# Kernel optimization log

Measured on AMD Instinct MI355X. Metric: run time of the kernel, lower is better.

## Reference

```python
import jax, jax.numpy as jnp
import numpy as np

NEG_INF = -9e15
ALPHA = 2.0  # LeakyReLU negative slope from init (alpha=2)


def setup_inputs() -> dict:
    key = jax.random.key(0)
    k1, k2, k3, k4 = jax.random.split(key, 4)
    B, N, Fin, Fout = 8, 2048, 256, 128
    x = jax.random.normal(k1, (B, N, Fin), dtype=jnp.float32)
    adj = jax.random.randint(k2, (B, N, N), 0, 2, dtype=jnp.int32)
    # xavier_uniform with gain=1.414
    def xavier(k, shape, gain=1.414):
        fan_in, fan_out = shape[0], shape[1]
        bound = gain * np.sqrt(6.0 / (fan_in + fan_out))
        return jax.random.uniform(k, shape, jnp.float32, -bound, bound)
    W = xavier(k3, (Fin, Fout))
    a = xavier(k4, (2 * Fout, 1))
    return {"x": x, "adj": adj, "W": W, "a": a}


def reference(x, adj, W, a):
    # Wh: [B, N, Fout]
    Wh = jnp.matmul(x, W)
    Fout = W.shape[1]
    a1 = a[:Fout, 0]   # [Fout]
    a2 = a[Fout:, 0]   # [Fout]
    f1 = jnp.einsum('bnf,f->bn', Wh, a1)  # [B, N]
    f2 = jnp.einsum('bnf,f->bn', Wh, a2)  # [B, N]
    e = f1[:, :, None] + f2[:, None, :]   # [B, N, N]
    e = jnp.where(e >= 0, e, ALPHA * e)   # leaky relu, slope 2
    e = jnp.where(adj > 0, e, NEG_INF)
    attention = jax.nn.softmax(e, axis=2)
    # dropout: eval mode (no-op)
    h_prime = jnp.matmul(attention, Wh)   # [B, N, Fout]
    # concat=True -> elu
    return jnp.where(h_prime > 0, h_prime, jnp.expm1(h_prime))
```

## Files before the change

kernel.cpp:

```cpp
#include <hip/hip_runtime.h>
#include <hip/hip_bf16.h>
#include <math.h>

#define NEGINF (-9000000000000000.0f)

constexpr int B_   = 8;
constexpr int N_   = 2048;
constexpr int FIN  = 256;
constexpr int FOUT = 128;

constexpr int CH  = 512;
constexpr int NCH = N_ / CH;
constexpr int PR  = CH + 8;
constexpr int XR  = FIN + 8;
constexpr int TR  = 40;

typedef __attribute__((ext_vector_type(8))) short bf16x8;
typedef __attribute__((ext_vector_type(4))) float f32x4;

static __device__ __forceinline__ unsigned short f2bf(float f) {
    __hip_bfloat16 h = __float2bfloat16(f);
    return *reinterpret_cast<unsigned short*>(&h);
}

__global__ __launch_bounds__(256) void k0_wt(const float* __restrict__ W,
                                             unsigned short* __restrict__ Wt) {
    const int n = blockIdx.x;
    const int k = threadIdx.x;
    Wt[n * FIN + k] = f2bf(W[k * FOUT + n]);
}

__global__ __launch_bounds__(256) void kadj(const int* __restrict__ adj,
                                            unsigned long long* __restrict__ mask) {
    const int tid  = threadIdx.x;
    const int wave = tid >> 6, lane = tid & 63;
    const size_t row = (size_t)blockIdx.x * 4 + wave;
    const int* src = adj + row * N_;
    unsigned long long* dst = mask + row * (N_ / 64);
#pragma unroll
    for (int g = 0; g < 4; ++g) {
        unsigned long long m[8];
#pragma unroll
        for (int q = 0; q < 8; ++q)
            m[q] = __ballot(src[g * 512 + q * 64 + lane] > 0);
        unsigned long long v = m[0];
#pragma unroll
        for (int q = 1; q < 8; ++q) v = (lane == q) ? m[q] : v;
        if (lane < 8) dst[g * 8 + lane] = v;
    }
}

__global__ __launch_bounds__(256) void ka_wh(const float* __restrict__ x,
                                             const unsigned short* __restrict__ Wt,
                                             const float* __restrict__ a,
                                             unsigned short* __restrict__ WhT,
                                             float* __restrict__ f1,
                                             float* __restrict__ f2) {
    __shared__ unsigned short xs[32 * XR];
    __shared__ float as[2 * FOUT];
    __shared__ float fred[2][4][32];

    const int tid = threadIdx.x;
    const int j0  = blockIdx.x * 32;
    const int b   = j0 >> 11;
    const int jb  = j0 & (N_ - 1);

    if (tid < 2 * FOUT) as[tid] = a[tid];
    {
        const float4* xsrc = (const float4*)(x + (size_t)j0 * FIN);
#pragma unroll
        for (int t = 0; t < 8; ++t) {
            const int idx = tid + t * 256;
            float4 v = xsrc[idx];
            const int row = idx >> 6, c4 = idx & 63;
            ushort4 u;
            u.x = f2bf(v.x); u.y = f2bf(v.y); u.z = f2bf(v.z); u.w = f2bf(v.w);
            *(ushort4*)&xs[row * XR + c4 * 4] = u;
        }
    }
    __syncthreads();

    const int wave = tid >> 6, lane = tid & 63;
    const int quad = lane >> 4, l16 = lane & 15;

    f32x4 acc[2][2];
#pragma unroll
    for (int aa = 0; aa < 2; ++aa)
#pragma unroll
        for (int nn = 0; nn < 2; ++nn) acc[aa][nn] = {0.f, 0.f, 0.f, 0.f};

    const unsigned short* wtA0 = Wt + (size_t)(32 * wave + l16) * FIN;
    const unsigned short* wtA1 = wtA0 + 16 * FIN;
#pragma unroll
    for (int ks = 0; ks < FIN / 32; ++ks) {
        const int kof = ks * 32 + quad * 8;
        bf16x8 af0 = *(const bf16x8*)&wtA0[kof];
        bf16x8 af1 = *(const bf16x8*)&wtA1[kof];
        bf16x8 bf0 = *(const bf16x8*)&xs[l16 * XR + kof];
        bf16x8 bf1 = *(const bf16x8*)&xs[(16 + l16) * XR + kof];
        acc[0][0] = __builtin_amdgcn_mfma_f32_16x16x32_bf16(af0, bf0, acc[0][0], 0, 0, 0);
        acc[0][1] = __builtin_amdgcn_mfma_f32_16x16x32_bf16(af0, bf1, acc[0][1], 0, 0, 0);
        acc[1][0] = __builtin_amdgcn_mfma_f32_16x16x32_bf16(af1, bf0, acc[1][0], 0, 0, 0);
        acc[1][1] = __builtin_amdgcn_mfma_f32_16x16x32_bf16(af1, bf1, acc[1][1], 0, 0, 0);
    }
    __syncthreads();

    unsigned short* T = xs;
    float pf[2][2] = {{0.f, 0.f}, {0.f, 0.f}};
#pragma unroll
    for (int aa = 0; aa < 2; ++aa)
#pragma unroll
        for (int nn = 0; nn < 2; ++nn)
#pragma unroll
            for (int r = 0; r < 4; ++r) {
                const int d = 32 * wave + 16 * aa + 4 * quad + r;
                const float v = acc[aa][nn][r];
                T[d * TR + nn * 16 + l16] = f2bf(v);
                pf[0][nn] += v * as[d];
                pf[1][nn] += v * as[FOUT + d];
            }
#pragma unroll
    for (int ff = 0; ff < 2; ++ff)
#pragma unroll
        for (int nn = 0; nn < 2; ++nn) {
            float v = pf[ff][nn];
            v += __shfl_xor(v, 16);
            v += __shfl_xor(v, 32);
            pf[ff][nn] = v;
        }
    if (quad == 0) {
#pragma unroll
        for (int ff = 0; ff < 2; ++ff)
#pragma unroll
            for (int nn = 0; nn < 2; ++nn)
                fred[ff][wave][nn * 16 + l16] = pf[ff][nn];
    }
    __syncthreads();

    unsigned short* dstW = WhT + (size_t)b * FOUT * N_;
#pragma unroll
    for (int it = 0; it < 2; ++it) {
        const int idx = it * 256 + tid;
        const int d = idx >> 2, q = idx & 3;
        bf16x8 v = *(const bf16x8*)&T[d * TR + q * 8];
        *(bf16x8*)&dstW[(size_t)d * N_ + jb + q * 8] = v;
    }
    if (tid < 64) {
        const int ff = tid >> 5, j32 = tid & 31;
        const float s = fred[ff][0][j32] + fred[ff][1][j32] +
                        fred[ff][2][j32] + fred[ff][3][j32];
        (ff ? f2 : f1)[(size_t)b * N_ + jb + j32] = s;
    }
}

__global__ __launch_bounds__(256) void kb_attn(const unsigned int* __restrict__ mask32,
                                               const unsigned short* __restrict__ WhT,
                                               const float* __restrict__ f1,
                                               const float* __restrict__ f2,
                                               float* __restrict__ out) {
    __shared__ unsigned short p[16 * PR];
    __shared__ float alpha_s[16];
    __shared__ float rsum[16];

    const int tid  = threadIdx.x;
    const int b    = blockIdx.x & 7;
    const int i0   = (blockIdx.x >> 3) * 16;
    const int wave = tid >> 6, lane = tid & 63;
    const int quad = lane >> 4, l16 = lane & 15;

    const float4* f2b4 = (const float4*)(f2 + (size_t)b * N_);

    float f1r[4], m_run[4], s_run[4];
#pragma unroll
    for (int rr = 0; rr < 4; ++rr) {
        f1r[rr]   = f1[(size_t)b * N_ + i0 + wave * 4 + rr];
        m_run[rr] = NEGINF;
        s_run[rr] = 0.f;
    }

    f32x4 acc0 = {0.f, 0.f, 0.f, 0.f}, acc1 = {0.f, 0.f, 0.f, 0.f};
    const int n0 = wave * 32;
    const unsigned short* wB0 = WhT + (size_t)b * FOUT * N_ + (size_t)(n0 + l16) * N_;
    const unsigned short* wB1 = wB0 + (size_t)16 * N_;
    const unsigned short* pA  = &p[l16 * PR];

    for (int c = 0; c < NCH; ++c) {
#pragma unroll
        for (int rr = 0; rr < 4; ++rr) {
            const int ti = wave * 4 + rr;
            const int i  = i0 + ti;
            const float f1i = f1r[rr];
            const unsigned int* mrow =
                mask32 + ((size_t)b * N_ + i) * (N_ / 32);
            const unsigned int w0 = mrow[c * 16 + (lane >> 3)];
            const unsigned int w1 = mrow[c * 16 + 8 + (lane >> 3)];
            const unsigned int t0 = (w0 >> ((lane & 7) * 4)) & 0xF;
            const unsigned int t1 = (w1 >> ((lane & 7) * 4)) & 0xF;
            const int c4 = c * (CH / 4);
            float4 fv0 = f2b4[c4 + lane];
            float4 fv1 = f2b4[c4 + 64 + lane];

            float e[8];
            e[0] = f1i + fv0.x; e[1] = f1i + fv0.y; e[2] = f1i + fv0.z; e[3] = f1i + fv0.w;
            e[4] = f1i + fv1.x; e[5] = f1i + fv1.y; e[6] = f1i + fv1.z; e[7] = f1i + fv1.w;
#pragma unroll
            for (int q = 0; q < 8; ++q) e[q] = (e[q] >= 0.f) ? e[q] : 2.f * e[q];
#pragma unroll
            for (int q = 0; q < 4; ++q) {
                if (!((t0 >> q) & 1)) e[q]     = NEGINF;
                if (!((t1 >> q) & 1)) e[4 + q] = NEGINF;
            }

            float mx = e[0];
#pragma unroll
            for (int q = 1; q < 8; ++q) mx = fmaxf(mx, e[q]);
#pragma unroll
            for (int o = 32; o; o >>= 1) mx = fmaxf(mx, __shfl_xor(mx, o));

            const float mnew = fmaxf(m_run[rr], mx);
            const float al   = __expf(m_run[rr] - mnew);
            float pv[8];
            float s8 = 0.f;
#pragma unroll
            for (int q = 0; q < 8; ++q) { pv[q] = __expf(e[q] - mnew); s8 += pv[q]; }
#pragma unroll
            for (int o = 32; o; o >>= 1) s8 += __shfl_xor(s8, o);
            s_run[rr] = s_run[rr] * al + s8;
            m_run[rr] = mnew;

            ushort4 u0, u1;
            u0.x = f2bf(pv[0]); u0.y = f2bf(pv[1]); u0.z = f2bf(pv[2]); u0.w = f2bf(pv[3]);
            u1.x = f2bf(pv[4]); u1.y = f2bf(pv[5]); u1.z = f2bf(pv[6]); u1.w = f2bf(pv[7]);
            *(ushort4*)&p[ti * PR + 4 * lane]       = u0;
            *(ushort4*)&p[ti * PR + 256 + 4 * lane] = u1;
            if (lane == 0) alpha_s[ti] = al;
            if (c == NCH - 1 && lane == 0) rsum[ti] = s_run[rr];
        }
        __syncthreads();

#pragma unroll
        for (int r = 0; r < 4; ++r) {
            const float alr = alpha_s[quad * 4 + r];
            acc0[r] *= alr;
            acc1[r] *= alr;
        }
        const int kbase = c * CH;
#pragma unroll
        for (int ks = 0; ks < CH / 32; ++ks) {
            const int kof = ks * 32 + quad * 8;
            bf16x8 afr = *(const bf16x8*)&pA[kof];
            bf16x8 b0  = *(const bf16x8*)&wB0[kbase + kof];
            bf16x8 b1  = *(const bf16x8*)&wB1[kbase + kof];
            acc0 = __builtin_amdgcn_mfma_f32_16x16x32_bf16(afr, b0, acc0, 0, 0, 0);
            acc1 = __builtin_amdgcn_mfma_f32_16x16x32_bf16(afr, b1, acc1, 0, 0, 0);
        }
        __syncthreads();
    }

#pragma unroll
    for (int r = 0; r < 4; ++r) {
        const int m = quad * 4 + r;
        const float inv = 1.f / rsum[m];
        float v0 = acc0[r] * inv;
        float v1 = acc1[r] * inv;
        v0 = (v0 > 0.f) ? v0 : expm1f(v0);
        v1 = (v1 > 0.f) ? v1 : expm1f(v1);
        const size_t base = ((size_t)b * N_ + i0 + m) * FOUT + n0;
        out[base + l16]      = v0;
        out[base + 16 + l16] = v1;
    }
}

extern "C" void kernel_launch(void* const* d_in, const int* in_sizes, int n_in,
                              void* d_out, int out_size, void* d_ws, size_t ws_size,
                              hipStream_t stream) {
    const float* x   = (const float*)d_in[0];
    const int*   adj = (const int*)d_in[1];
    const float* W   = (const float*)d_in[2];
    const float* a   = (const float*)d_in[3];
    float* out = (float*)d_out;

    unsigned short* WhT = (unsigned short*)d_ws;
    unsigned short* Wt  = WhT + (size_t)B_ * FOUT * N_;
    float* f1 = (float*)(Wt + (size_t)FOUT * FIN);
    float* f2 = f1 + (size_t)B_ * N_;
    unsigned long long* mask = (unsigned long long*)(f2 + (size_t)B_ * N_);

    hipLaunchKernelGGL(kadj, dim3(B_ * N_ / 4), dim3(256), 0, stream, adj, mask);
    hipLaunchKernelGGL(k0_wt, dim3(FOUT), dim3(FIN), 0, stream, W, Wt);
    hipLaunchKernelGGL(ka_wh, dim3(B_ * N_ / 32), dim3(256), 0, stream,
                       x, Wt, a, WhT, f1, f2);
    hipLaunchKernelGGL(kb_attn, dim3(B_ * N_ / 16), dim3(256), 0, stream,
                       (const unsigned int*)mask, WhT, f1, f2, out);
}
```

Baseline: 285.7 us.

## Fuse adjacency read into attention kernel, drop running max, double-buffer P tile

Removes the separate kernel that packed the int32 adjacency into a bitmask. The attention kernel now reads adj directly with nontemporal vector loads and zeroes masked probabilities. The online-softmax max tracking and rescaling are dropped, so exp is taken on raw scores and only a sum is kept. P is double-buffered in shared memory so the next chunk's scores are computed before the current chunk's MFMA work. Dropping the max subtraction relies on scores staying small enough not to overflow exp, and a fully masked row would give a divide by zero.

```diff
diff --git a/kernel.cpp b/kernel.cpp
--- a/kernel.cpp
+++ b/kernel.cpp
@@ -1,8 +1,6 @@
 #include <hip/hip_runtime.h>
 #include <hip/hip_bf16.h>
 #include <math.h>
-
-#define NEGINF (-9000000000000000.0f)
 
 constexpr int B_   = 8;
 constexpr int N_   = 2048;
@@ -17,10 +15,14 @@
 
 typedef __attribute__((ext_vector_type(8))) short bf16x8;
 typedef __attribute__((ext_vector_type(4))) float f32x4;
+typedef __attribute__((ext_vector_type(4))) int   i32x4;
 
 static __device__ __forceinline__ unsigned short f2bf(float f) {
     __hip_bfloat16 h = __float2bfloat16(f);
     return *reinterpret_cast<unsigned short*>(&h);
+}
+static __device__ __forceinline__ i32x4 ntload4(const int* p) {
+    return __builtin_nontemporal_load((const i32x4*)p);
 }
 
 __global__ __launch_bounds__(256) void k0_wt(const float* __restrict__ W,
@@ -28,26 +30,6 @@
     const int n = blockIdx.x;
     const int k = threadIdx.x;
     Wt[n * FIN + k] = f2bf(W[k * FOUT + n]);
-}
-
-__global__ __launch_bounds__(256) void kadj(const int* __restrict__ adj,
-                                            unsigned long long* __restrict__ mask) {
-    const int tid  = threadIdx.x;
-    const int wave = tid >> 6, lane = tid & 63;
-    const size_t row = (size_t)blockIdx.x * 4 + wave;
-    const int* src = adj + row * N_;
-    unsigned long long* dst = mask + row * (N_ / 64);
-#pragma unroll
-    for (int g = 0; g < 4; ++g) {
-        unsigned long long m[8];
-#pragma unroll
-        for (int q = 0; q < 8; ++q)
-            m[q] = __ballot(src[g * 512 + q * 64 + lane] > 0);
-        unsigned long long v = m[0];
-#pragma unroll
-        for (int q = 1; q < 8; ++q) v = (lane == q) ? m[q] : v;
-        if (lane < 8) dst[g * 8 + lane] = v;
-    }
 }
 
 __global__ __launch_bounds__(256) void ka_wh(const float* __restrict__ x,
@@ -153,13 +135,56 @@
     }
 }
 
-__global__ __launch_bounds__(256) void kb_attn(const unsigned int* __restrict__ mask32,
+static __device__ __forceinline__ void kb_phaseA(
+    const int c, const int lane, const int wave, const int i0,
+    const int* __restrict__ adjB, const float4* __restrict__ f2b4,
+    const float* __restrict__ f1r, float* __restrict__ s_run,
+    unsigned short* __restrict__ pb)
+{
+    const float4 fv0 = f2b4[c * (CH / 4) + lane];
+    const float4 fv1 = f2b4[c * (CH / 4) + 64 + lane];
+#pragma unroll
+    for (int rr = 0; rr < 4; ++rr) {
+        const int ti = wave * 4 + rr;
+        const int i  = i0 + ti;
+        const int* arow = adjB + (size_t)i * N_ + c * CH;
+        const i32x4 av0 = ntload4(arow + 4 * lane);
+        const i32x4 av1 = ntload4(arow + 256 + 4 * lane);
+        const float f1i = f1r[rr];
+
+        float e[8];
+        e[0] = f1i + fv0.x; e[1] = f1i + fv0.y; e[2] = f1i + fv0.z; e[3] = f1i + fv0.w;
+        e[4] = f1i + fv1.x; e[5] = f1i + fv1.y; e[6] = f1i + fv1.z; e[7] = f1i + fv1.w;
+#pragma unroll
+        for (int q = 0; q < 8; ++q) e[q] = (e[q] >= 0.f) ? e[q] : 2.f * e[q];
+
+        float pv[8];
+        pv[0] = (av0.x > 0) ? __expf(e[0]) : 0.f;
+        pv[1] = (av0.y > 0) ? __expf(e[1]) : 0.f;
+        pv[2] = (av0.z > 0) ? __expf(e[2]) : 0.f;
+        pv[3] = (av0.w > 0) ? __expf(e[3]) : 0.f;
+        pv[4] = (av1.x > 0) ? __expf(e[4]) : 0.f;
+        pv[5] = (av1.y > 0) ? __expf(e[5]) : 0.f;
+        pv[6] = (av1.z > 0) ? __expf(e[6]) : 0.f;
+        pv[7] = (av1.w > 0) ? __expf(e[7]) : 0.f;
+
+        s_run[rr] += ((pv[0] + pv[1]) + (pv[2] + pv[3])) +
+                     ((pv[4] + pv[5]) + (pv[6] + pv[7]));
+
+        ushort4 u0, u1;
+        u0.x = f2bf(pv[0]); u0.y = f2bf(pv[1]); u0.z = f2bf(pv[2]); u0.w = f2bf(pv[3]);
+        u1.x = f2bf(pv[4]); u1.y = f2bf(pv[5]); u1.z = f2bf(pv[6]); u1.w = f2bf(pv[7]);
+        *(ushort4*)&pb[ti * PR + 4 * lane]       = u0;
+        *(ushort4*)&pb[ti * PR + 256 + 4 * lane] = u1;
+    }
+}
+
+__global__ __launch_bounds__(256) void kb_attn(const int* __restrict__ adj,
                                                const unsigned short* __restrict__ WhT,
                                                const float* __restrict__ f1,
                                                const float* __restrict__ f2,
                                                float* __restrict__ out) {
-    __shared__ unsigned short p[16 * PR];
-    __shared__ float alpha_s[16];
+    __shared__ unsigned short p[2][16 * PR];
     __shared__ float rsum[16];
 
     const int tid  = threadIdx.x;
@@ -169,12 +194,12 @@
     const int quad = lane >> 4, l16 = lane & 15;
 
     const float4* f2b4 = (const float4*)(f2 + (size_t)b * N_);
-
-    float f1r[4], m_run[4], s_run[4];
+    const int*    adjB = adj + (size_t)b * N_ * N_;
+
+    float f1r[4], s_run[4];
 #pragma unroll
     for (int rr = 0; rr < 4; ++rr) {
         f1r[rr]   = f1[(size_t)b * N_ + i0 + wave * 4 + rr];
-        m_run[rr] = NEGINF;
         s_run[rr] = 0.f;
     }
 
@@ -182,68 +207,25 @@
     const int n0 = wave * 32;
     const unsigned short* wB0 = WhT + (size_t)b * FOUT * N_ + (size_t)(n0 + l16) * N_;
     const unsigned short* wB1 = wB0 + (size_t)16 * N_;
-    const unsigned short* pA  = &p[l16 * PR];
+
+    kb_phaseA(0, lane, wave, i0, adjB, f2b4, f1r, s_run, &p[0][0]);
+    __syncthreads();
 
     for (int c = 0; c < NCH; ++c) {
-#pragma unroll
-        for (int rr = 0; rr < 4; ++rr) {
-            const int ti = wave * 4 + rr;
-            const int i  = i0 + ti;
-            const float f1i = f1r[rr];
-            const unsigned int* mrow =
-                mask32 + ((size_t)b * N_ + i) * (N_ / 32);
-            const unsigned int w0 = mrow[c * 16 + (lane >> 3)];
-            const unsigned int w1 = mrow[c * 16 + 8 + (lane >> 3)];
-            const unsigned int t0 = (w0 >> ((lane & 7) * 4)) & 0xF;
-            const unsigned int t1 = (w1 >> ((lane & 7) * 4)) & 0xF;
-            const int c4 = c * (CH / 4);
-            float4 fv0 = f2b4[c4 + lane];
-            float4 fv1 = f2b4[c4 + 64 + lane];
-
-            float e[8];
-            e[0] = f1i + fv0.x; e[1] = f1i + fv0.y; e[2] = f1i + fv0.z; e[3] = f1i + fv0.w;
-            e[4] = f1i + fv1.x; e[5] = f1i + fv1.y; e[6] = f1i + fv1.z; e[7] = f1i + fv1.w;
-#pragma unroll
-            for (int q = 0; q < 8; ++q) e[q] = (e[q] >= 0.f) ? e[q] : 2.f * e[q];
-#pragma unroll
-            for (int q = 0; q < 4; ++q) {
-                if (!((t0 >> q) & 1)) e[q]     = NEGINF;
-                if (!((t1 >> q) & 1)) e[4 + q] = NEGINF;
+        if (c + 1 < NCH) {
+            kb_phaseA(c + 1, lane, wave, i0, adjB, f2b4, f1r, s_run,
+                      &p[(c + 1) & 1][0]);
+        } else {
+#pragma unroll
+            for (int rr = 0; rr < 4; ++rr) {
+                float s = s_run[rr];
+#pragma unroll
+                for (int o = 32; o; o >>= 1) s += __shfl_xor(s, o);
+                if (lane == 0) rsum[wave * 4 + rr] = s;
             }
-
-            float mx = e[0];
-#pragma unroll
-            for (int q = 1; q < 8; ++q) mx = fmaxf(mx, e[q]);
-#pragma unroll
-            for (int o = 32; o; o >>= 1) mx = fmaxf(mx, __shfl_xor(mx, o));
-
-            const float mnew = fmaxf(m_run[rr], mx);
-            const float al   = __expf(m_run[rr] - mnew);
-            float pv[8];
-            float s8 = 0.f;
-#pragma unroll
-            for (int q = 0; q < 8; ++q) { pv[q] = __expf(e[q] - mnew); s8 += pv[q]; }
-#pragma unroll
-            for (int o = 32; o; o >>= 1) s8 += __shfl_xor(s8, o);
-            s_run[rr] = s_run[rr] * al + s8;
-            m_run[rr] = mnew;
-
-            ushort4 u0, u1;
-            u0.x = f2bf(pv[0]); u0.y = f2bf(pv[1]); u0.z = f2bf(pv[2]); u0.w = f2bf(pv[3]);
-            u1.x = f2bf(pv[4]); u1.y = f2bf(pv[5]); u1.z = f2bf(pv[6]); u1.w = f2bf(pv[7]);
-            *(ushort4*)&p[ti * PR + 4 * lane]       = u0;
-            *(ushort4*)&p[ti * PR + 256 + 4 * lane] = u1;
-            if (lane == 0) alpha_s[ti] = al;
-            if (c == NCH - 1 && lane == 0) rsum[ti] = s_run[rr];
-        }
-        __syncthreads();
-
-#pragma unroll
-        for (int r = 0; r < 4; ++r) {
-            const float alr = alpha_s[quad * 4 + r];
-            acc0[r] *= alr;
-            acc1[r] *= alr;
-        }
+        }
+
+        const unsigned short* pA = &p[c & 1][l16 * PR];
         const int kbase = c * CH;
 #pragma unroll
         for (int ks = 0; ks < CH / 32; ++ks) {
@@ -284,12 +266,10 @@
     unsigned short* Wt  = WhT + (size_t)B_ * FOUT * N_;
     float* f1 = (float*)(Wt + (size_t)FOUT * FIN);
     float* f2 = f1 + (size_t)B_ * N_;
-    unsigned long long* mask = (unsigned long long*)(f2 + (size_t)B_ * N_);
-
-    hipLaunchKernelGGL(kadj, dim3(B_ * N_ / 4), dim3(256), 0, stream, adj, mask);
+
     hipLaunchKernelGGL(k0_wt, dim3(FOUT), dim3(FIN), 0, stream, W, Wt);
     hipLaunchKernelGGL(ka_wh, dim3(B_ * N_ / 32), dim3(256), 0, stream,
                        x, Wt, a, WhT, f1, f2);
     hipLaunchKernelGGL(kb_attn, dim3(B_ * N_ / 16), dim3(256), 0, stream,
-                       (const unsigned int*)mask, WhT, f1, f2, out);
-}
+                       adj, WhT, f1, f2, out);
+}
```

Result: faster. 260.6 us (-8.8%).
